# Kernel tuning notes

Measured on AMD Instinct MI355X. Metric: run time of the kernel, lower is better.

Reference implementation:

```python
import jax, jax.numpy as jnp
import numpy as np

L, H, LATENT, DM, DH, FF = 4, 4, 256, 768, 192, 1024
EPS = 1e-6      # fast_transformers RecurrentLinearAttention eps
LN_EPS = 1e-5


def make_pe(d_model=LATENT, max_len=5000):
    pos = np.arange(max_len, dtype=np.float32)[:, None]
    div = np.exp(np.arange(0, d_model, 2, dtype=np.float32) * (-np.log(10000.0) / d_model))
    pe = np.zeros((max_len, d_model), np.float32)
    pe[:, 0::2] = np.sin(pos * div)
    pe[:, 1::2] = np.cos(pos * div)
    return jnp.asarray(pe)

PE = make_pe()


def layer_norm(x, g, b):
    m = x.mean(-1, keepdims=True)
    v = ((x - m) ** 2).mean(-1, keepdims=True)
    return (x - m) * jax.lax.rsqrt(v + LN_EPS) * g + b


def setup_inputs() -> dict:
    key = jax.random.key(0)
    ks = jax.random.split(key, 16)
    bs, nj, nf, T, A, C = 8, 25, 6, 80, 6, 12
    s = 0.02
    return dict(
        x=jax.random.normal(ks[0], (bs, nj, nf, T), jnp.float32),
        y=jax.random.randint(ks[1], (bs, A), 0, C),
        ind_map=jnp.sort(jax.random.randint(ks[2], (T, bs), 0, A), axis=0),
        act_tstamps=jnp.sort(jax.random.randint(ks[3], (bs, A), 1, T + 1), axis=1).at[:, -1].set(T),
        skel_W=jax.random.normal(ks[4], (nj * nf, LATENT), jnp.float32) * s,
        skel_b=jnp.zeros((LATENT,), jnp.float32),
        muQuery=jax.random.normal(ks[5], (C, LATENT), jnp.float32),
        sigmaQuery=jax.random.normal(ks[6], (C, LATENT), jnp.float32),
        Wq=jax.random.normal(ks[7], (L, DM, DM), jnp.float32) * s,
        bq=jnp.zeros((L, DM), jnp.float32),
        Wk=jax.random.normal(ks[8], (L, DM, DM), jnp.float32) * s,
        bk=jnp.zeros((L, DM), jnp.float32),
        Wv=jax.random.normal(ks[9], (L, DM, DM), jnp.float32) * s,
        bv=jnp.zeros((L, DM), jnp.float32),
        Wo=jax.random.normal(ks[10], (L, DM, DM), jnp.float32) * s,
        bo=jnp.zeros((L, DM), jnp.float32),
        W1=jax.random.normal(ks[11], (L, DM, FF), jnp.float32) * s,
        b1=jnp.zeros((L, FF), jnp.float32),
        W2=jax.random.normal(ks[12], (L, FF, DM), jnp.float32) * s,
        b2=jnp.zeros((L, DM), jnp.float32),
        ln1_g=jnp.ones((L, DM), jnp.float32), ln1_b=jnp.zeros((L, DM), jnp.float32),
        ln2_g=jnp.ones((L, DM), jnp.float32), ln2_b=jnp.zeros((L, DM), jnp.float32),
        lnf_g=jnp.ones((DM,), jnp.float32), lnf_b=jnp.zeros((DM,), jnp.float32),
    )


def _fwd(x, y, ind_map, act_tstamps, skel_W, skel_b, muQuery, sigmaQuery,
         Wq, bq, Wk, bk, Wv, bv, Wo, bo, W1, b1, W2, b2,
         ln1_g, ln1_b, ln2_g, ln2_b, lnf_g, lnf_b):
    bs, nj, nf, T = x.shape
    # skeleton embedding: [T, bs, njoints*nfeats] @ W -> [T, bs, LATENT]
    xe = x.transpose(3, 0, 1, 2).reshape(T, bs, nj * nf) @ skel_W + skel_b
    mu_q = muQuery[y]        # [bs, A, LATENT]
    sig_q = sigmaQuery[y]
    barange = jnp.arange(bs)

    @jax.checkpoint
    def step(carry, inputs):
        S, Z = carry                         # [L,bs,H,DH,DH], [L,bs,H,DH]
        t, xt, ind_t = inputs
        cm = mu_q[barange, ind_t]            # gather per-sample current action query
        cs = sig_q[barange, ind_t]
        xseq = jnp.stack([cm, cs, xt], 0)    # [3, bs, LATENT]
        start = jnp.where(t == 0, 0, t + 2)  # PositionalEncoding(last_pos=t, offset=2)
        pe3 = jax.lax.dynamic_slice_in_dim(PE, start, 3, 0)
        xseq = xseq + pe3[:, None, :]
        h = xseq.transpose(1, 0, 2).reshape(bs, 3 * LATENT)  # flatten -> [bs, DM]
        nS, nZ = [], []
        for l in range(L):
            q = (h @ Wq[l] + bq[l]).reshape(bs, H, DH)
            k = (h @ Wk[l] + bk[l]).reshape(bs, H, DH)
            v = (h @ Wv[l] + bv[l]).reshape(bs, H, DH)
            Q = jax.nn.elu(q) + 1.0          # linear-attention feature map
            K = jax.nn.elu(k) + 1.0
            Sl = S[l] + K[..., :, None] * v[..., None, :]   # state update S += k (x) v
            Zl = Z[l] + K
            inv = 1.0 / (jnp.einsum('bhd,bhd->bh', Q, Zl) + EPS)
            att = jnp.einsum('bhd,bhdm,bh->bhm', Q, Sl, inv).reshape(bs, DM)
            h1 = layer_norm(h + att @ Wo[l] + bo[l], ln1_g[l], ln1_b[l])
            ffn = jax.nn.relu(h1 @ W1[l] + b1[l]) @ W2[l] + b2[l]
            h = layer_norm(h1 + ffn, ln2_g[l], ln2_b[l])
            nS.append(Sl); nZ.append(Zl)
        h = layer_norm(h, lnf_g, lnf_b)      # encoder final norm
        return (jnp.stack(nS), jnp.stack(nZ)), h

    S0 = jnp.zeros((L, bs, H, DH, DH), x.dtype)
    Z0 = jnp.zeros((L, bs, H, DH), x.dtype)
    _, finals = jax.lax.scan(step, (S0, Z0), (jnp.arange(T), xe, ind_map))  # finals: [T,bs,DM]
    tsel = jnp.maximum(act_tstamps - 1, 0)                       # [bs, A]
    mu = finals[:, :, :LATENT][tsel, barange[:, None]]           # [bs, A, LATENT]
    logvar = finals[:, :, LATENT:2 * LATENT][tsel, barange[:, None]]
    return mu, logvar


def reference(x, y, ind_map, act_tstamps, skel_W, skel_b, muQuery, sigmaQuery,
              Wq, bq, Wk, bk, Wv, bv, Wo, bo, W1, b1, W2, b2,
              ln1_g, ln1_b, ln2_g, ln2_b, lnf_g, lnf_b):
    return _fwd(x, y, ind_map, act_tstamps, skel_W, skel_b, muQuery, sigmaQuery,
                Wq, bq, Wk, bk, Wv, bv, Wo, bo, W1, b1, W2, b2,
                ln1_g, ln1_b, ln2_g, ln2_b, lnf_g, lnf_b)
```

## Files before the change

### kernel.cpp

```cpp
#include <hip/hip_runtime.h>
#include <math.h>

#define TT 80
#define BS 8
#define NA 6
#define DMODEL 768
#define NH 4
#define DH 192
#define FFD 1024
#define NROWS (TT*BS)
#define NQKV (3*DMODEL)

typedef __bf16 bf16;
typedef __bf16 bf16x8 __attribute__((ext_vector_type(8)));
typedef float  f32x4  __attribute__((ext_vector_type(4)));

__device__ __forceinline__ float block_reduce_sum256(float v, float* sm4) {
#pragma unroll
    for (int off = 32; off > 0; off >>= 1) v += __shfl_down(v, off, 64);
    int lane = threadIdx.x & 63, wid = threadIdx.x >> 6;
    if (lane == 0) sm4[wid] = v;
    __syncthreads();
    float r = sm4[0] + sm4[1] + sm4[2] + sm4[3];
    __syncthreads();
    return r;
}

__global__ __launch_bounds__(256) void embed_k(
        const float* __restrict__ x, const int* __restrict__ y,
        const int* __restrict__ ind_map, const float* __restrict__ skel_W,
        const float* __restrict__ skel_b, const float* __restrict__ muQ,
        const float* __restrict__ sigQ, float* __restrict__ h0,
        bf16* __restrict__ h0b) {
    __shared__ float xrow[152];
    int r = blockIdx.x;
    int t = r >> 3, b = r & 7;
    int c = threadIdx.x;
    if (c < 150) xrow[c] = x[(b * 150 + c) * TT + t];
    __syncthreads();
    float acc = skel_b[c];
    for (int jf = 0; jf < 150; jf++) acc += xrow[jf] * skel_W[jf * 256 + c];
    int ind_t = ind_map[t * 8 + b];
    int yb = y[b * NA + ind_t];
    float cm = muQ[yb * 256 + c];
    float cs = sigQ[yb * 256 + c];
    int start = (t == 0) ? 0 : (t + 2);
    float div = expf((float)(c & ~1) * (-9.210340371976184f / 256.0f));
    float p0, p1, p2;
    if (c & 1) {
        p0 = cosf((float)start * div);
        p1 = cosf((float)(start + 1) * div);
        p2 = cosf((float)(start + 2) * div);
    } else {
        p0 = sinf((float)start * div);
        p1 = sinf((float)(start + 1) * div);
        p2 = sinf((float)(start + 2) * div);
    }
    float* hr = h0 + (size_t)r * DMODEL;
    float v0 = cm + p0, v1 = cs + p1, v2 = acc + p2;
    hr[c] = v0; hr[c + 256] = v1; hr[c + 512] = v2;
    bf16* hb = h0b + (size_t)r * DMODEL;
    hb[c] = (bf16)v0; hb[c + 256] = (bf16)v1; hb[c + 512] = (bf16)v2;
}

__global__ __launch_bounds__(256) void transpose_k(
        const float* __restrict__ Wq, const float* __restrict__ Wk,
        const float* __restrict__ Wv, const float* __restrict__ Wo,
        const float* __restrict__ W1, const float* __restrict__ W2,
        bf16* __restrict__ qkvT, bf16* __restrict__ woT,
        bf16* __restrict__ w1T, bf16* __restrict__ w2T) {
    int lz = blockIdx.z;
    int l = lz >> 2, z = lz & 3;
    int K = (z == 3) ? 1024 : 768;
    int N = (z == 0) ? 2304 : (z == 2) ? 1024 : 768;
    int k0 = blockIdx.x * 32, n0 = blockIdx.y * 32;
    if (k0 >= K || n0 >= N) return;
    const float* src; bf16* dst; int ldsrc; int ncol;
    if (z == 0) {
        if (n0 < 768)       { src = Wq + (size_t)l * 768 * 768; ncol = n0; }
        else if (n0 < 1536) { src = Wk + (size_t)l * 768 * 768; ncol = n0 - 768; }
        else                { src = Wv + (size_t)l * 768 * 768; ncol = n0 - 1536; }
        dst = qkvT + (size_t)l * NQKV * DMODEL; ldsrc = 768;
    } else if (z == 1) { src = Wo + (size_t)l * 768 * 768;  dst = woT + (size_t)l * 768 * 768;  ldsrc = 768;  ncol = n0; }
    else if (z == 2)   { src = W1 + (size_t)l * 768 * 1024; dst = w1T + (size_t)l * 1024 * 768; ldsrc = 1024; ncol = n0; }
    else               { src = W2 + (size_t)l * 1024 * 768; dst = w2T + (size_t)l * 768 * 1024; ldsrc = 768;  ncol = n0; }
    __shared__ float tile[32][33];
    int tx = threadIdx.x & 31, ty = threadIdx.x >> 5;
#pragma unroll
    for (int i = 0; i < 4; i++) {
        int r = ty + 8 * i;
        tile[r][tx] = src[(size_t)(k0 + r) * ldsrc + ncol + tx];
    }
    __syncthreads();
#pragma unroll
    for (int i = 0; i < 4; i++) {
        int r = ty + 8 * i;
        dst[(size_t)(n0 + r) * K + k0 + tx] = (bf16)tile[tx][r];
    }
}

template <int EPI>
__global__ __launch_bounds__(256) void gemm_mfma(
        const bf16* __restrict__ A, const bf16* __restrict__ Bt,
        const float* __restrict__ bias_q, const float* __restrict__ bias_k,
        const float* __restrict__ bias_v, const float* __restrict__ resid,
        float* __restrict__ outF, bf16* __restrict__ outB,
        int M, int N, int K) {
    __shared__ __attribute__((aligned(16))) bf16 As0[64][40];
    __shared__ __attribute__((aligned(16))) bf16 As1[64][40];
    __shared__ __attribute__((aligned(16))) bf16 Bs0[64][40];
    __shared__ __attribute__((aligned(16))) bf16 Bs1[64][40];
    int tid = threadIdx.x;
    int m0 = blockIdx.y * 64, n0 = blockIdx.x * 64;
    int w = tid >> 6;
    int l = tid & 63;
    int lm = l & 15, lq = l >> 4;
    int sr = tid >> 2;
    int sk = (tid & 3) * 8;
    const bf16* Arow = &A[(size_t)(m0 + sr) * K];
    const bf16* Brow = &Bt[(size_t)(n0 + sr) * K];
    f32x4 acc[4] = {};
    uint4 a0 = *(const uint4*)&Arow[sk];
    uint4 a1 = *(const uint4*)&Arow[32 + sk];
    uint4 b0 = *(const uint4*)&Brow[sk];
    uint4 b1 = *(const uint4*)&Brow[32 + sk];
    for (int k0 = 0; k0 < K; k0 += 64) {
        __syncthreads();
        *(uint4*)&As0[sr][sk] = a0;
        *(uint4*)&As1[sr][sk] = a1;
        *(uint4*)&Bs0[sr][sk] = b0;
        *(uint4*)&Bs1[sr][sk] = b1;
        __syncthreads();
        int k2 = k0 + 64; if (k2 >= K) k2 = 0;
        a0 = *(const uint4*)&Arow[k2 + sk];
        a1 = *(const uint4*)&Arow[k2 + 32 + sk];
        b0 = *(const uint4*)&Brow[k2 + sk];
        b1 = *(const uint4*)&Brow[k2 + 32 + sk];
        bf16x8 af0 = *(bf16x8*)&As0[w * 16 + lm][lq * 8];
        bf16x8 af1 = *(bf16x8*)&As1[w * 16 + lm][lq * 8];
#pragma unroll
        for (int nb = 0; nb < 4; nb++) {
            bf16x8 bf0 = *(bf16x8*)&Bs0[nb * 16 + lm][lq * 8];
            acc[nb] = __builtin_amdgcn_mfma_f32_16x16x32_bf16(af0, bf0, acc[nb], 0, 0, 0);
        }
#pragma unroll
        for (int nb = 0; nb < 4; nb++) {
            bf16x8 bf1 = *(bf16x8*)&Bs1[nb * 16 + lm][lq * 8];
            acc[nb] = __builtin_amdgcn_mfma_f32_16x16x32_bf16(af1, bf1, acc[nb], 0, 0, 0);
        }
    }
#pragma unroll
    for (int nb = 0; nb < 4; nb++) {
        int col = n0 + nb * 16 + lm;
        float b;
        bool do_elu = false;
        if (EPI == 0) {
            if (col < 768)       { b = bias_q[col];        do_elu = true; }
            else if (col < 1536) { b = bias_k[col - 768];  do_elu = true; }
            else                 { b = bias_v[col - 1536]; }
        } else {
            b = bias_q[col];
        }
#pragma unroll
        for (int r = 0; r < 4; r++) {
            int row = m0 + w * 16 + lq * 4 + r;
            float v = acc[nb][r] + b;
            if (EPI == 0) {
                if (do_elu) v = (v > 0.0f) ? (v + 1.0f) : expf(v);
                outB[(size_t)row * N + col] = (bf16)v;
            } else if (EPI == 1) {
                v += resid[(size_t)row * N + col];
                outF[(size_t)row * N + col] = v;
            } else {
                v = fmaxf(v, 0.0f);
                outB[(size_t)row * N + col] = (bf16)v;
            }
        }
    }
}

__global__ __launch_bounds__(256) void ln_k(
        const float* __restrict__ in, float* __restrict__ outF,
        bf16* __restrict__ outB,
        const float* __restrict__ g, const float* __restrict__ b) {
    int wave = threadIdx.x >> 6, lane = threadIdx.x & 63;
    int row = blockIdx.x * 4 + wave;
    const float* xr = in + (size_t)row * DMODEL;
    float4 v[3];
    float s = 0.0f;
#pragma unroll
    for (int j = 0; j < 3; j++) {
        v[j] = *(const float4*)&xr[lane * 4 + 256 * j];
        s += v[j].x + v[j].y + v[j].z + v[j].w;
    }
#pragma unroll
    for (int mk = 1; mk < 64; mk <<= 1) s += __shfl_xor(s, mk, 64);
    float m = s * (1.0f / 768.0f);
    float sq = 0.0f;
#pragma unroll
    for (int j = 0; j < 3; j++) {
        v[j].x -= m; v[j].y -= m; v[j].z -= m; v[j].w -= m;
        sq += v[j].x * v[j].x + v[j].y * v[j].y + v[j].z * v[j].z + v[j].w * v[j].w;
    }
#pragma unroll
    for (int mk = 1; mk < 64; mk <<= 1) sq += __shfl_xor(sq, mk, 64);
    float r = rsqrtf(sq * (1.0f / 768.0f) + 1e-5f);
    float* orow = outF + (size_t)row * DMODEL;
    bf16* brow = outB + (size_t)row * DMODEL;
#pragma unroll
    for (int j = 0; j < 3; j++) {
        int c = lane * 4 + 256 * j;
        float4 gg = *(const float4*)&g[c];
        float4 bb = *(const float4*)&b[c];
        float o0 = v[j].x * r * gg.x + bb.x;
        float o1 = v[j].y * r * gg.y + bb.y;
        float o2 = v[j].z * r * gg.z + bb.z;
        float o3 = v[j].w * r * gg.w + bb.w;
        *(float4*)&orow[c] = make_float4(o0, o1, o2, o3);
        bf16 tmp4[4] = {(bf16)o0, (bf16)o1, (bf16)o2, (bf16)o3};
        *(uint2*)&brow[c] = *(uint2*)tmp4;
    }
}

__global__ __launch_bounds__(320) void attn_k(
        const bf16* __restrict__ qkvB, bf16* __restrict__ att) {
    __shared__ __attribute__((aligned(16))) char smem[64000];
    bf16* Qs = (bf16*)smem;
    bf16* Ks = (bf16*)(smem + 32000);
    bf16* Aij = (bf16*)smem;
    bf16* VT = (bf16*)(smem + 16640);

    int b = blockIdx.x >> 2, h = blockIdx.x & 3;
    int tid = threadIdx.x;
    int w = tid >> 6, l = tid & 63;
    int lm = l & 15, lq = l >> 4;

    uint4 vreg[6];
#pragma unroll
    for (int u = 0; u < 6; u++) {
        int c = tid + 320 * u;
        int t = c / 24, cc = c % 24;
        int d0 = cc * 8;
        size_t g = (size_t)(t * 8 + b) * NQKV + h * DH + d0;
        uint4 qv = *(const uint4*)&qkvB[g];
        uint4 kv = *(const uint4*)&qkvB[g + 768];
        vreg[u]  = *(const uint4*)&qkvB[g + 1536];
        *(uint4*)&Qs[t * 200 + d0] = qv;
        *(uint4*)&Ks[t * 200 + d0] = kv;
    }
    __syncthreads();

    f32x4 acc[5] = {};
#pragma unroll
    for (int k0 = 0; k0 < 192; k0 += 32) {
        bf16x8 af = *(bf16x8*)&Qs[(w * 16 + lm) * 200 + lq * 8 + k0];
#pragma unroll
        for (int nb = 0; nb < 5; nb++) {
            bf16x8 bfr = *(bf16x8*)&Ks[(nb * 16 + lm) * 200 + lq * 8 + k0];
            acc[nb] = __builtin_amdgcn_mfma_f32_16x16x32_bf16(af, bfr, acc[nb], 0, 0, 0);
        }
    }
    float mval[5][4];
    float rs[4] = {0.f, 0.f, 0.f, 0.f};
#pragma unroll
    for (int nb = 0; nb < 5; nb++)
#pragma unroll
        for (int r = 0; r < 4; r++) {
            int t = w * 16 + lq * 4 + r, tau = nb * 16 + lm;
            float v = (tau <= t) ? acc[nb][r] : 0.0f;
            mval[nb][r] = v;
            rs[r] += v;
        }
#pragma unroll
    for (int mk = 1; mk < 16; mk <<= 1)
#pragma unroll
        for (int r = 0; r < 4; r++) rs[r] += __shfl_xor(rs[r], mk, 64);
    float inv[4];
#pragma unroll
    for (int r = 0; r < 4; r++) inv[r] = 1.0f / (rs[r] + 1e-6f);

    __syncthreads();

#pragma unroll
    for (int nb = 0; nb < 5; nb++)
#pragma unroll
        for (int r = 0; r < 4; r++)
            Aij[(w * 16 + lq * 4 + r) * 104 + nb * 16 + lm] = (bf16)mval[nb][r];
    *(uint2*)&Aij[(tid >> 2) * 104 + 80 + (tid & 3) * 4] = make_uint2(0u, 0u);
#pragma unroll
    for (int u = 0; u < 6; u++) {
        int c = tid + 320 * u;
        int t = c / 24, cc = c % 24;
        int d0 = cc * 8;
        bf16 tmp8[8];
        *(uint4*)tmp8 = vreg[u];
#pragma unroll
        for (int j = 0; j < 8; j++) VT[(d0 + j) * 104 + t] = tmp8[j];
    }
    if (tid < 192) {
        *(uint4*)&VT[tid * 104 + 80] = make_uint4(0u, 0u, 0u, 0u);
        *(uint4*)&VT[tid * 104 + 88] = make_uint4(0u, 0u, 0u, 0u);
    }
    __syncthreads();

#pragma unroll 1
    for (int nc = 0; nc < 12; nc++) {
        f32x4 a2 = {};
#pragma unroll
        for (int k0 = 0; k0 < 96; k0 += 32) {
            bf16x8 af = *(bf16x8*)&Aij[(w * 16 + lm) * 104 + lq * 8 + k0];
            bf16x8 bfr = *(bf16x8*)&VT[(nc * 16 + lm) * 104 + lq * 8 + k0];
            a2 = __builtin_amdgcn_mfma_f32_16x16x32_bf16(af, bfr, a2, 0, 0, 0);
        }
#pragma unroll
        for (int r = 0; r < 4; r++) {
            int t = w * 16 + lq * 4 + r;
            att[(size_t)(t * 8 + b) * DMODEL + h * DH + nc * 16 + lm] =
                (bf16)(a2[r] * inv[r]);
        }
    }
}

__global__ __launch_bounds__(256) void final_k(
        const float* __restrict__ h, const int* __restrict__ act_ts,
        const float* __restrict__ g, const float* __restrict__ bb,
        float* __restrict__ out) {
    __shared__ float sm4[4];
    int ba = blockIdx.x;
    int b = ba / NA;
    int ts = act_ts[ba];
    int t = ts - 1; if (t < 0) t = 0;
    const float* xr = h + (size_t)(t * 8 + b) * DMODEL;
    int c = threadIdx.x;
    float x0 = xr[c], x1 = xr[c + 256], x2 = xr[c + 512];
    float m = block_reduce_sum256(x0 + x1 + x2, sm4) * (1.0f / 768.0f);
    float d0 = x0 - m, d1 = x1 - m, d2 = x2 - m;
    float v = block_reduce_sum256(d0 * d0 + d1 * d1 + d2 * d2, sm4) * (1.0f / 768.0f);
    float r = rsqrtf(v + 1e-5f);
    out[ba * 256 + c]            = d0 * r * g[c] + bb[c];
    out[48 * 256 + ba * 256 + c] = d1 * r * g[c + 256] + bb[c + 256];
}

extern "C" void kernel_launch(void* const* d_in, const int* in_sizes, int n_in,
                              void* d_out, int out_size, void* d_ws, size_t ws_size,
                              hipStream_t stream) {
    const float* x       = (const float*)d_in[0];
    const int*   y       = (const int*)d_in[1];
    const int*   ind_map = (const int*)d_in[2];
    const int*   act_ts  = (const int*)d_in[3];
    const float* skel_W  = (const float*)d_in[4];
    const float* skel_b  = (const float*)d_in[5];
    const float* muQ     = (const float*)d_in[6];
    const float* sigQ    = (const float*)d_in[7];
    const float* Wq = (const float*)d_in[8];   const float* bq = (const float*)d_in[9];
    const float* Wk = (const float*)d_in[10];  const float* bk = (const float*)d_in[11];
    const float* Wv = (const float*)d_in[12];  const float* bv = (const float*)d_in[13];
    const float* Wo = (const float*)d_in[14];  const float* bo = (const float*)d_in[15];
    const float* W1 = (const float*)d_in[16];  const float* b1 = (const float*)d_in[17];
    const float* W2 = (const float*)d_in[18];  const float* b2 = (const float*)d_in[19];
    const float* ln1_g = (const float*)d_in[20]; const float* ln1_b = (const float*)d_in[21];
    const float* ln2_g = (const float*)d_in[22]; const float* ln2_b = (const float*)d_in[23];
    const float* lnf_g = (const float*)d_in[24]; const float* lnf_b = (const float*)d_in[25];
    float* out = (float*)d_out;

    char* p = (char*)d_ws;
    const size_t R  = (size_t)NROWS * DMODEL;
    float* h    = (float*)p; p += R * 4;
    float* h1   = (float*)p; p += R * 4;
    float* tmp  = (float*)p; p += R * 4;
    bf16* qkvB  = (bf16*)p;  p += (size_t)NROWS * NQKV * 2;
    bf16* hB    = (bf16*)p;  p += R * 2;
    bf16* h1B   = (bf16*)p;  p += R * 2;
    bf16* attB  = (bf16*)p;  p += R * 2;
    bf16* ffn1B = (bf16*)p;  p += (size_t)NROWS * FFD * 2;
    bf16* qkvT  = (bf16*)p;  p += (size_t)4 * NQKV * DMODEL * 2;
    bf16* woT   = (bf16*)p;  p += (size_t)4 * DMODEL * DMODEL * 2;
    bf16* w1T   = (bf16*)p;  p += (size_t)4 * FFD * DMODEL * 2;
    bf16* w2T   = (bf16*)p;  p += (size_t)4 * DMODEL * FFD * 2;

    dim3 gT(32, 72, 16);
    transpose_k<<<gT, 256, 0, stream>>>(Wq, Wk, Wv, Wo, W1, W2, qkvT, woT, w1T, w2T);
    embed_k<<<NROWS, 256, 0, stream>>>(x, y, ind_map, skel_W, skel_b, muQ, sigQ, h, hB);

    dim3 gQKV(NQKV / 64, 10);
    dim3 g768(12, 10);
    dim3 g1024(16, 10);
    for (int l = 0; l < 4; l++) {
        const bf16* qkvTl = qkvT + (size_t)l * NQKV * DMODEL;
        const bf16* woTl  = woT  + (size_t)l * DMODEL * DMODEL;
        const bf16* w1Tl  = w1T  + (size_t)l * FFD * DMODEL;
        const bf16* w2Tl  = w2T  + (size_t)l * DMODEL * FFD;
        gemm_mfma<0><<<gQKV, 256, 0, stream>>>(hB, qkvTl,
                bq + l * DMODEL, bk + l * DMODEL, bv + l * DMODEL,
                nullptr, nullptr, qkvB, NROWS, NQKV, DMODEL);
        attn_k<<<32, 320, 0, stream>>>(qkvB, attB);
        gemm_mfma<1><<<g768, 256, 0, stream>>>(attB, woTl,
                bo + l * DMODEL, nullptr, nullptr, h, tmp, nullptr,
                NROWS, DMODEL, DMODEL);
        ln_k<<<NROWS / 4, 256, 0, stream>>>(tmp, h1, h1B, ln1_g + l * DMODEL, ln1_b + l * DMODEL);
        gemm_mfma<2><<<g1024, 256, 0, stream>>>(h1B, w1Tl,
                b1 + l * FFD, nullptr, nullptr, nullptr, nullptr, ffn1B,
                NROWS, FFD, DMODEL);
        gemm_mfma<1><<<g768, 256, 0, stream>>>(ffn1B, w2Tl,
                b2 + l * DMODEL, nullptr, nullptr, h1, tmp, nullptr,
                NROWS, DMODEL, FFD);
        ln_k<<<NROWS / 4, 256, 0, stream>>>(tmp, h, hB, ln2_g + l * DMODEL, ln2_b + l * DMODEL);
    }

    final_k<<<48, 256, 0, stream>>>(h, act_ts, lnf_g, lnf_b, out);
}
```

Measured before the change: 423.6 us.

## Merge weight transpose with embedding and split attention output across blocks

The weight transpose and embedding kernels are merged into one flat-grid prep kernel, which removes a launch and drops the old grid's early-exit blocks. The attention kernel now launches three blocks per (batch, head), and each block computes the A·V output for a third of the head dimension, so 96 blocks run instead of 32. The cost is that each attention block redoes the QK^T scores, softmax and V transpose, tripling that part of the work and the qkv loads.

New measurement: 418.8 us. Within noise of the previous version (-1.1%).

```diff
diff --git a/kernel.cpp b/kernel.cpp
--- a/kernel.cpp
+++ b/kernel.cpp
@@ -26,76 +26,87 @@
     return r;
 }
 
-__global__ __launch_bounds__(256) void embed_k(
+__global__ __launch_bounds__(256) void prep_k(
         const float* __restrict__ x, const int* __restrict__ y,
-        const int* __restrict__ ind_map, const float* __restrict__ skel_W,
-        const float* __restrict__ skel_b, const float* __restrict__ muQ,
-        const float* __restrict__ sigQ, float* __restrict__ h0,
-        bf16* __restrict__ h0b) {
-    __shared__ float xrow[152];
-    int r = blockIdx.x;
-    int t = r >> 3, b = r & 7;
-    int c = threadIdx.x;
-    if (c < 150) xrow[c] = x[(b * 150 + c) * TT + t];
-    __syncthreads();
-    float acc = skel_b[c];
-    for (int jf = 0; jf < 150; jf++) acc += xrow[jf] * skel_W[jf * 256 + c];
-    int ind_t = ind_map[t * 8 + b];
-    int yb = y[b * NA + ind_t];
-    float cm = muQ[yb * 256 + c];
-    float cs = sigQ[yb * 256 + c];
-    int start = (t == 0) ? 0 : (t + 2);
-    float div = expf((float)(c & ~1) * (-9.210340371976184f / 256.0f));
-    float p0, p1, p2;
-    if (c & 1) {
-        p0 = cosf((float)start * div);
-        p1 = cosf((float)(start + 1) * div);
-        p2 = cosf((float)(start + 2) * div);
-    } else {
-        p0 = sinf((float)start * div);
-        p1 = sinf((float)(start + 1) * div);
-        p2 = sinf((float)(start + 2) * div);
-    }
-    float* hr = h0 + (size_t)r * DMODEL;
-    float v0 = cm + p0, v1 = cs + p1, v2 = acc + p2;
-    hr[c] = v0; hr[c + 256] = v1; hr[c + 512] = v2;
-    bf16* hb = h0b + (size_t)r * DMODEL;
-    hb[c] = (bf16)v0; hb[c + 256] = (bf16)v1; hb[c + 512] = (bf16)v2;
-}
-
-__global__ __launch_bounds__(256) void transpose_k(
+        const int* __restrict__ ind_map,
+        const float* __restrict__ skel_W, const float* __restrict__ skel_b,
+        const float* __restrict__ muQ, const float* __restrict__ sigQ,
         const float* __restrict__ Wq, const float* __restrict__ Wk,
         const float* __restrict__ Wv, const float* __restrict__ Wo,
         const float* __restrict__ W1, const float* __restrict__ W2,
         bf16* __restrict__ qkvT, bf16* __restrict__ woT,
-        bf16* __restrict__ w1T, bf16* __restrict__ w2T) {
-    int lz = blockIdx.z;
-    int l = lz >> 2, z = lz & 3;
-    int K = (z == 3) ? 1024 : 768;
-    int N = (z == 0) ? 2304 : (z == 2) ? 1024 : 768;
-    int k0 = blockIdx.x * 32, n0 = blockIdx.y * 32;
-    if (k0 >= K || n0 >= N) return;
-    const float* src; bf16* dst; int ldsrc; int ncol;
-    if (z == 0) {
-        if (n0 < 768)       { src = Wq + (size_t)l * 768 * 768; ncol = n0; }
-        else if (n0 < 1536) { src = Wk + (size_t)l * 768 * 768; ncol = n0 - 768; }
-        else                { src = Wv + (size_t)l * 768 * 768; ncol = n0 - 1536; }
-        dst = qkvT + (size_t)l * NQKV * DMODEL; ldsrc = 768;
-    } else if (z == 1) { src = Wo + (size_t)l * 768 * 768;  dst = woT + (size_t)l * 768 * 768;  ldsrc = 768;  ncol = n0; }
-    else if (z == 2)   { src = W1 + (size_t)l * 768 * 1024; dst = w1T + (size_t)l * 1024 * 768; ldsrc = 1024; ncol = n0; }
-    else               { src = W2 + (size_t)l * 1024 * 768; dst = w2T + (size_t)l * 768 * 1024; ldsrc = 768;  ncol = n0; }
+        bf16* __restrict__ w1T, bf16* __restrict__ w2T,
+        float* __restrict__ h0, bf16* __restrict__ h0b) {
     __shared__ float tile[32][33];
-    int tx = threadIdx.x & 31, ty = threadIdx.x >> 5;
-#pragma unroll
-    for (int i = 0; i < 4; i++) {
-        int r = ty + 8 * i;
-        tile[r][tx] = src[(size_t)(k0 + r) * ldsrc + ncol + tx];
-    }
-    __syncthreads();
-#pragma unroll
-    for (int i = 0; i < 4; i++) {
-        int r = ty + 8 * i;
-        dst[(size_t)(n0 + r) * K + k0 + tx] = (bf16)tile[tx][r];
+    __shared__ float xrow[152];
+    int bid = blockIdx.x, tid = threadIdx.x;
+    if (bid < 15360) {
+        const float* src; bf16* dst; int ldsrc, Kd, n0, k0;
+        int l = bid / 3840, r = bid % 3840;
+        if (r < 1728) {
+            int kt = r % 24, nt = r / 24;
+            k0 = kt * 32; n0 = nt * 32; Kd = 768; ldsrc = 768;
+            dst = qkvT + (size_t)l * NQKV * DMODEL;
+            if (n0 < 768)       { src = Wq + (size_t)l * 589824 + n0; }
+            else if (n0 < 1536) { src = Wk + (size_t)l * 589824 + (n0 - 768); }
+            else                { src = Wv + (size_t)l * 589824 + (n0 - 1536); }
+        } else if (r < 2304) {
+            int r2 = r - 1728; int kt = r2 % 24, nt = r2 / 24;
+            k0 = kt * 32; n0 = nt * 32; Kd = 768; ldsrc = 768;
+            src = Wo + (size_t)l * 589824 + n0;
+            dst = woT + (size_t)l * 589824;
+        } else if (r < 3072) {
+            int r2 = r - 2304; int kt = r2 % 24, nt = r2 / 24;
+            k0 = kt * 32; n0 = nt * 32; Kd = 768; ldsrc = 1024;
+            src = W1 + (size_t)l * 786432 + n0;
+            dst = w1T + (size_t)l * 786432;
+        } else {
+            int r2 = r - 3072; int kt = r2 % 32, nt = r2 / 32;
+            k0 = kt * 32; n0 = nt * 32; Kd = 1024; ldsrc = 768;
+            src = W2 + (size_t)l * 786432 + n0;
+            dst = w2T + (size_t)l * 786432;
+        }
+        int tx = tid & 31, ty = tid >> 5;
+#pragma unroll
+        for (int i = 0; i < 4; i++) {
+            int rr = ty + 8 * i;
+            tile[rr][tx] = src[(size_t)(k0 + rr) * ldsrc + tx];
+        }
+        __syncthreads();
+#pragma unroll
+        for (int i = 0; i < 4; i++) {
+            int rr = ty + 8 * i;
+            dst[(size_t)(n0 + rr) * Kd + k0 + tx] = (bf16)tile[tx][rr];
+        }
+    } else {
+        int r = bid - 15360;
+        int t = r >> 3, b = r & 7;
+        int c = tid;
+        if (c < 150) xrow[c] = x[(b * 150 + c) * TT + t];
+        __syncthreads();
+        float acc = skel_b[c];
+        for (int jf = 0; jf < 150; jf++) acc += xrow[jf] * skel_W[jf * 256 + c];
+        int ind_t = ind_map[t * 8 + b];
+        int yb = y[b * NA + ind_t];
+        float cm = muQ[yb * 256 + c];
+        float cs = sigQ[yb * 256 + c];
+        int start = (t == 0) ? 0 : (t + 2);
+        float div = expf((float)(c & ~1) * (-9.210340371976184f / 256.0f));
+        float p0, p1, p2;
+        if (c & 1) {
+            p0 = cosf((float)start * div);
+            p1 = cosf((float)(start + 1) * div);
+            p2 = cosf((float)(start + 2) * div);
+        } else {
+            p0 = sinf((float)start * div);
+            p1 = sinf((float)(start + 1) * div);
+            p2 = sinf((float)(start + 2) * div);
+        }
+        float* hr = h0 + (size_t)r * DMODEL;
+        float v0 = cm + p0, v1 = cs + p1, v2 = acc + p2;
+        hr[c] = v0; hr[c + 256] = v1; hr[c + 512] = v2;
+        bf16* hb = h0b + (size_t)r * DMODEL;
+        hb[c] = (bf16)v0; hb[c + 256] = (bf16)v1; hb[c + 512] = (bf16)v2;
     }
 }
 
@@ -229,8 +240,8 @@
     bf16* Ks = (bf16*)(smem + 32000);
     bf16* Aij = (bf16*)smem;
     bf16* VT = (bf16*)(smem + 16640);
-
-    int b = blockIdx.x >> 2, h = blockIdx.x & 3;
+    int bh = blockIdx.x / 3, part = blockIdx.x % 3;
+    int bb = bh >> 2, hd = bh & 3;
     int tid = threadIdx.x;
     int w = tid >> 6, l = tid & 63;
     int lm = l & 15, lq = l >> 4;
@@ -241,7 +252,7 @@
         int c = tid + 320 * u;
         int t = c / 24, cc = c % 24;
         int d0 = cc * 8;
-        size_t g = (size_t)(t * 8 + b) * NQKV + h * DH + d0;
+        size_t g = (size_t)(t * 8 + bb) * NQKV + hd * DH + d0;
         uint4 qv = *(const uint4*)&qkvB[g];
         uint4 kv = *(const uint4*)&qkvB[g + 768];
         vreg[u]  = *(const uint4*)&qkvB[g + 1536];
@@ -304,7 +315,7 @@
     __syncthreads();
 
 #pragma unroll 1
-    for (int nc = 0; nc < 12; nc++) {
+    for (int nc = part * 4; nc < part * 4 + 4; nc++) {
         f32x4 a2 = {};
 #pragma unroll
         for (int k0 = 0; k0 < 96; k0 += 32) {
@@ -315,7 +326,7 @@
 #pragma unroll
         for (int r = 0; r < 4; r++) {
             int t = w * 16 + lq * 4 + r;
-            att[(size_t)(t * 8 + b) * DMODEL + h * DH + nc * 16 + lm] =
+            att[(size_t)(t * 8 + bb) * DMODEL + hd * DH + nc * 16 + lm] =
                 (bf16)(a2[r] * inv[r]);
         }
     }
@@ -378,9 +389,9 @@
     bf16* w1T   = (bf16*)p;  p += (size_t)4 * FFD * DMODEL * 2;
     bf16* w2T   = (bf16*)p;  p += (size_t)4 * DMODEL * FFD * 2;
 
-    dim3 gT(32, 72, 16);
-    transpose_k<<<gT, 256, 0, stream>>>(Wq, Wk, Wv, Wo, W1, W2, qkvT, woT, w1T, w2T);
-    embed_k<<<NROWS, 256, 0, stream>>>(x, y, ind_map, skel_W, skel_b, muQ, sigQ, h, hB);
+    prep_k<<<16000, 256, 0, stream>>>(x, y, ind_map, skel_W, skel_b, muQ, sigQ,
+                                      Wq, Wk, Wv, Wo, W1, W2,
+                                      qkvT, woT, w1T, w2T, h, hB);
 
     dim3 gQKV(NQKV / 64, 10);
     dim3 g768(12, 10);
@@ -393,7 +404,7 @@
         gemm_mfma<0><<<gQKV, 256, 0, stream>>>(hB, qkvTl,
                 bq + l * DMODEL, bk + l * DMODEL, bv + l * DMODEL,
                 nullptr, nullptr, qkvB, NROWS, NQKV, DMODEL);
-        attn_k<<<32, 320, 0, stream>>>(qkvB, attB);
+        attn_k<<<96, 320, 0, stream>>>(qkvB, attB);
         gemm_mfma<1><<<g768, 256, 0, stream>>>(attB, woTl,
                 bo + l * DMODEL, nullptr, nullptr, h, tmp, nullptr,
                 NROWS, DMODEL, DMODEL);
```
